# Kernel optimization log

Hardware: AMD Instinct MI355X
Metric: run time of the kernel (lower is better)

The kernel has to match this reference:

```python
import jax, jax.numpy as jnp
import numpy as np

B, CS, CD = 2, 128, 128
SRC = (8, 16, 16)
DST = (16, 32, 32)
G, K = 8, 3           # deform_groups, dcn_kernel
K3 = K ** 3


def setup_inputs() -> dict:
    key = jax.random.key(0)
    k1, k2, k3, k4 = jax.random.split(key, 4)
    feat_1x_src = jax.random.normal(k1, (B, CS) + SRC, dtype=jnp.float32)
    feat_2x_dst = jax.random.normal(k2, (B, CD) + DST, dtype=jnp.float32)
    # 1x1 Conv3d (bias=False): in = CD + CS = 256, out = K^3 * 3 * G = 648
    w_offset = jax.random.normal(k3, (K3 * 3 * G, CD + CS), dtype=jnp.float32) * 0.02
    # DeformConv3D weight: [Cout, Cin, K, K, K], no bias
    w_dcn = jax.random.normal(k4, (CD, CS, K, K, K), dtype=jnp.float32) * 0.05
    return {"feat_1x_src": feat_1x_src, "feat_2x_dst": feat_2x_dst,
            "w_offset": w_offset, "w_dcn": w_dcn}


def _trilinear_gather(x_flat, z, y, x, Di, Hi, Wi):
    """Zero-padded trilinear sampling.
    x_flat: [B,G,Cg,Din*Hin*Win]; z,y,x: [B,G,P] float coords. -> [B,G,Cg,P]"""
    z0 = jnp.floor(z); y0 = jnp.floor(y); x0 = jnp.floor(x)
    fz = z - z0; fy = y - y0; fx = x - x0
    z0i = z0.astype(jnp.int32); y0i = y0.astype(jnp.int32); x0i = x0.astype(jnp.int32)
    acc = jnp.zeros(x_flat.shape[:3] + (z.shape[-1],), x_flat.dtype)
    for dz in (0, 1):
        wz = fz if dz else 1.0 - fz
        iz = z0i + dz
        for dy in (0, 1):
            wy = fy if dy else 1.0 - fy
            iy = y0i + dy
            for dx in (0, 1):
                wx = fx if dx else 1.0 - fx
                ix = x0i + dx
                valid = ((iz >= 0) & (iz < Di) & (iy >= 0) & (iy < Hi)
                         & (ix >= 0) & (ix < Wi))
                idx = (jnp.clip(iz, 0, Di - 1) * (Hi * Wi)
                       + jnp.clip(iy, 0, Hi - 1) * Wi
                       + jnp.clip(ix, 0, Wi - 1))
                val = jnp.take_along_axis(x_flat, idx[:, :, None, :], axis=-1)
                acc = acc + val * (wz * wy * wx * valid)[:, :, None, :]
    return acc


def reference(feat_1x_src, feat_2x_dst, w_offset, w_dcn):
    b, cs = feat_1x_src.shape[:2]
    D, H, W = feat_2x_dst.shape[2:]
    cd = w_dcn.shape[0]
    # F.interpolate trilinear, align_corners=False (half-pixel == jax.image.resize)
    feat_up = jax.image.resize(feat_1x_src, (b, cs, D, H, W), method="trilinear")
    # 1x1 offset conv on concat([dst, 2*up])
    cat = jnp.concatenate([feat_2x_dst, feat_up * 2.0], axis=1)
    offset = jnp.einsum("bcdhw,oc->bodhw", cat, w_offset)
    # offsets: [B, G, K3, 3(z,y,x), D, H, W]
    off = offset.reshape(b, G, K3, 3, D, H, W)
    P = D * H * W
    Cg = cs // G
    x_flat = feat_up.reshape(b, G, Cg, P)
    dd, hh, ww = jnp.meshgrid(jnp.arange(D, dtype=jnp.float32),
                              jnp.arange(H, dtype=jnp.float32),
                              jnp.arange(W, dtype=jnp.float32), indexing="ij")
    pad = (K - 1) // 2
    taps = [(kz - pad, ky - pad, kx - pad)
            for kz in range(K) for ky in range(K) for kx in range(K)]
    samples = []
    for k, (kz, ky, kx) in enumerate(taps):
        z = (dd[None, None] + kz + off[:, :, k, 0]).reshape(b, G, P)
        y = (hh[None, None] + ky + off[:, :, k, 1]).reshape(b, G, P)
        x = (ww[None, None] + kx + off[:, :, k, 2]).reshape(b, G, P)
        samples.append(_trilinear_gather(x_flat, z, y, x, D, H, W).reshape(b, cs, P))
    samp = jnp.stack(samples, axis=2)           # [B, Cin, K3, P]
    wk = w_dcn.reshape(cd, cs, K3)
    out = jnp.einsum("bckp,ock->bop", samp, wk).reshape(b, cd, D, H, W)
    return jax.nn.relu(out)
```

## Files before the change

kernel.cpp:

```cpp
#include <hip/hip_runtime.h>
#include <hip/hip_fp16.h>
#include <math.h>

#define BB   2
#define CSN  128
#define CDN  128
#define SD   8
#define SH   16
#define SW   16
#define DD   16
#define DH   32
#define DW   32
#define PP   (DD*DH*DW)
#define GG   8
#define K3   27
#define OO   648

typedef _Float16 half8 __attribute__((ext_vector_type(8)));
typedef float f32x4 __attribute__((ext_vector_type(4)));

__global__ __launch_bounds__(256) void prep_kernel(
    const float* __restrict__ src, const float* __restrict__ wof,
    const float* __restrict__ wdcn, half8* __restrict__ uph8,
    half8* __restrict__ woxg, half8* __restrict__ wtx2)
{
    __shared__ float slab[2 * 8 * 16 * 17];
    const int bid = blockIdx.x;
    const int tid = threadIdx.x;

    if (bid < 512) {
        const int zo = bid & 15, pl = bid >> 4;
        const int h = pl & 1, g = (pl >> 1) & 7, b = pl >> 4;
        const int z0 = (zo - 1) >> 1;
        const float fz = (zo & 1) ? 0.25f : 0.75f;
        {
            const int zi = tid >> 7, cc = (tid >> 4) & 7, y = tid & 15;
            const int zsrc = min(max(z0 + zi, 0), SD - 1);
            const float* srow = src +
                (((size_t)(b * CSN + g * 16 + h * 8 + cc) * SD + zsrc) * SH + y) * SW;
            float* drow = &slab[((zi * 8 + cc) * 16 + y) * 17];
            *(float4*)(drow)      = *(const float4*)(srow);
            *(float4*)(drow + 4)  = *(const float4*)(srow + 4);
            *(float4*)(drow + 8)  = *(const float4*)(srow + 8);
            *(float4*)(drow + 12) = *(const float4*)(srow + 12);
        }
        __syncthreads();

        const float wz0 = 1.f - fz, wz1 = fz;
#pragma unroll 1
        for (int i = 0; i < 4; ++i) {
            const int pp = tid + i * 256;
            const int yo = pp >> 5, xo = pp & 31;
            const int y0 = (yo - 1) >> 1;
            const float fy = (yo & 1) ? 0.25f : 0.75f;
            const int ys0 = max(y0, 0), ys1 = min(y0 + 1, SH - 1);
            const int x0 = (xo - 1) >> 1;
            const float fx = (xo & 1) ? 0.25f : 0.75f;
            const int xs0 = max(x0, 0), xs1 = min(x0 + 1, SW - 1);
            const float w00 = (1.f - fy) * (1.f - fx), w01 = (1.f - fy) * fx;
            const float w10 = fy * (1.f - fx),         w11 = fy * fx;
            const int a00 = ys0 * 17 + xs0, a01 = ys0 * 17 + xs1;
            const int a10 = ys1 * 17 + xs0, a11 = ys1 * 17 + xs1;

            half8 hv;
#pragma unroll
            for (int cc = 0; cc < 8; ++cc) {
                const float* pa = &slab[(cc * 16) * 17];
                const float* pb = &slab[((8 + cc) * 16) * 17];
                const float s0 = w00 * pa[a00] + w01 * pa[a01]
                               + w10 * pa[a10] + w11 * pa[a11];
                const float s1 = w00 * pb[a00] + w01 * pb[a01]
                               + w10 * pb[a10] + w11 * pb[a11];
                hv[cc] = (_Float16)(wz0 * s0 + wz1 * s1);
            }
            uph8[(size_t)pl * PP + zo * 1024 + pp] = hv;
        }
    } else if (bid < 608) {
        const int i = (bid - 512) * 256 + tid;
        const int q = i & 3, lo = (i >> 2) & 15;
        const int t6 = i >> 6;
        const int ot = t6 % 6;
        const int gc0 = t6 / 6;
        const int c0 = gc0 & 7, g = gc0 >> 3;
        const int m = ot * 16 + lo;
        half8 hv;
#pragma unroll
        for (int j = 0; j < 8; ++j) hv[j] = (_Float16)0.0f;
        if (m < 81) {
            const int o = g * 81 + m;
            const int c = c0 * 32 + q * 8;
            const float sc = (c >= 128) ? 2.0f : 1.0f;
            const float* wr = wof + (size_t)o * 256 + c;
#pragma unroll
            for (int j = 0; j < 8; ++j) hv[j] = (_Float16)(wr[j] * sc);
        }
        woxg[i] = hv;
    } else {
        const int i = (bid - 608) * 256 + tid;
        const int q = i & 3, lo = (i >> 2) & 15, ot = (i >> 6) & 7;
        const int gp = i >> 9;
        const int pair = gp % 14, g = gp / 14;
        const int tap = pair * 2 + (q >> 1);
        half8 hv;
#pragma unroll
        for (int j = 0; j < 8; ++j) hv[j] = (_Float16)0.0f;
        if (tap < K3) {
            const int o = ot * 16 + lo;
            const int cb = g * 16 + (q & 1) * 8;
            const float* wr = wdcn + ((size_t)(o * CSN + cb)) * K3 + tap;
#pragma unroll
            for (int j = 0; j < 8; ++j) hv[j] = (_Float16)wr[(size_t)j * K3];
        }
        wtx2[i] = hv;
    }
}

#define REGB_OFF 32768
#define SH2_OFF  61568
#define LDS_TOTAL 78976
#define SROW 68

__global__ __launch_bounds__(512, 4) void mega_kernel(
    const float* __restrict__ dst, const float4* __restrict__ up4,
    const half8* __restrict__ woxg, const half8* __restrict__ wtx2,
    float* __restrict__ out)
{
    __shared__ __align__(16) char ldsraw[LDS_TOTAL];
    half8* catx = (half8*)ldsraw;
    char* regB = ldsraw + REGB_OFF;
    _Float16* offls = (_Float16*)(ldsraw + SH2_OFF);
    half8* sampx = (half8*)(ldsraw + SH2_OFF);

    const int tid = threadIdx.x;
    const int b = blockIdx.y;
    const int cb = blockIdx.x;
    const int X4 = (cb & 7) << 2, Y4 = ((cb >> 3) & 7) << 2, Z4 = (cb >> 6) << 2;

    {
        const int co = tid >> 4, pq = tid & 15;
        const int cz = pq >> 2, cy = pq & 3;
        const int pbase = ((Z4 + cz) << 10) + ((Y4 + cy) << 5) + X4;
        if (co < 16) {
            const int c = co * 8;
            const float* dp = dst + ((size_t)(b * CDN + c) << 14) + pbase;
            float vv[32];
#pragma unroll
            for (int j = 0; j < 8; ++j)
                *(float4*)&vv[j * 4] = *(const float4*)(dp + ((size_t)j << 14));
#pragma unroll
            for (int i = 0; i < 4; ++i) {
                half8 hh;
#pragma unroll
                for (int j = 0; j < 8; ++j) hh[j] = (_Float16)vv[j * 4 + i];
                catx[co * 64 + pq * 4 + i] = hh;
            }
        } else {
            const int g2 = (co - 16) >> 1, oct = (co - 16) & 1;
            const half8* u8 = (const half8*)up4;
            const size_t base =
                ((size_t)((b * GG + g2) * 2 + oct) << 14) + pbase;
#pragma unroll
            for (int i = 0; i < 4; ++i)
                catx[co * 64 + pq * 4 + i] = u8[base + i];
        }
    }

    const int w = tid >> 6, l = tid & 63, lo = l & 15, q = l >> 4;
    const int t2 = w >> 1, h = w & 1;
    const int tp = l;
    const int cz = tp >> 4, cy = (tp >> 2) & 3, cx = tp & 3;
    const int zoA = Z4 + cz, yoA = Y4 + cy, xoA = X4 + cx;

    f32x4 acc[4];
#pragma unroll
    for (int ps = 0; ps < 4; ++ps) acc[ps] = (f32x4){0.f, 0.f, 0.f, 0.f};

#pragma unroll 1
    for (int g = 0; g < 8; ++g) {
        __syncthreads();

#pragma unroll 1
        for (int c = tid; c < 1800; c += 512) {
            const int hf = c & 1;
            const int v = c >> 1;
            const int zz = v / 100, r2 = v - zz * 100;
            const int yy = r2 / 10, xx = r2 - yy * 10;
            const int vz = min(max(Z4 - 3 + zz, 0), DD - 1);
            const int vy = min(max(Y4 - 3 + yy, 0), DH - 1);
            const int vx = min(max(X4 - 3 + xx, 0), DW - 1);
            const float4 val =
                up4[(size_t)((b * GG + g) * 2 + hf) * PP +
                    (vz << 10) + (vy << 5) + vx];
            const int sw = (xx + yy + zz + hf) & 1;
            *(float4*)(regB + v * 32 + sw * 16) = val;
        }

        if (w < 6) {
            f32x4 a[4];
#pragma unroll
            for (int ps = 0; ps < 4; ++ps) a[ps] = (f32x4){0.f, 0.f, 0.f, 0.f};
#pragma unroll
            for (int c0 = 0; c0 < 8; ++c0) {
                const half8 A =
                    woxg[(size_t)((((g * 8 + c0) * 6 + w) * 16 + lo) * 4 + q)];
#pragma unroll
                for (int ps = 0; ps < 4; ++ps) {
                    const half8 B = catx[(c0 * 4 + q) * 64 + ps * 16 + lo];
                    a[ps] = __builtin_amdgcn_mfma_f32_16x16x32_f16(A, B, a[ps], 0, 0, 0);
                }
            }
#pragma unroll
            for (int ps = 0; ps < 4; ++ps) {
#pragma unroll
                for (int r = 0; r < 4; ++r) {
                    const int m = w * 16 + q * 4 + r;
                    if (m < 81)
                        offls[m * 64 + ps * 16 + lo] = (_Float16)a[ps][r];
                }
            }
        }
        __syncthreads();

        float offv[7][3];
#pragma unroll
        for (int r = 0; r < 7; ++r) {
            const int tap = r * 4 + t2;
            if (tap < K3) {
#pragma unroll
                for (int c = 0; c < 3; ++c)
                    offv[r][c] = (float)offls[(tap * 3 + c) * 64 + tp];
            }
        }
        __syncthreads();

#pragma unroll
        for (int r = 0; r < 7; ++r) {
            half8* dbuf = sampx + (r & 1) * 544;
            const int tap = r * 4 + t2;
            if (tap < K3) {
                const int kz = tap / 9 - 1;
                const int ky = (tap / 3) % 3 - 1;
                const int kx = (tap % 3) - 1;
                const float z = (float)(zoA + kz) + offv[r][0];
                const float y = (float)(yoA + ky) + offv[r][1];
                const float x = (float)(xoA + kx) + offv[r][2];
                const float zf = floorf(z), yf = floorf(y), xf = floorf(x);
                const float fz = z - zf, fy = y - yf, fx = x - xf;
                const int z0i = (int)zf, y0i = (int)yf, x0i = (int)xf;

                const float wz0 = ((unsigned)z0i < DD) ? 1.f - fz : 0.f;
                const float wz1 = ((unsigned)(z0i + 1) < DD) ? fz : 0.f;
                const float wy0 = ((unsigned)y0i < DH) ? 1.f - fy : 0.f;
                const float wy1 = ((unsigned)(y0i + 1) < DH) ? fy : 0.f;
                const float wx0 = ((unsigned)x0i < DW) ? 1.f - fx : 0.f;
                const float wx1 = ((unsigned)(x0i + 1) < DW) ? fx : 0.f;
                float wcs[8];
                wcs[0] = wz0 * wy0 * wx0; wcs[1] = wz0 * wy0 * wx1;
                wcs[2] = wz0 * wy1 * wx0; wcs[3] = wz0 * wy1 * wx1;
                wcs[4] = wz1 * wy0 * wx0; wcs[5] = wz1 * wy0 * wx1;
                wcs[6] = wz1 * wy1 * wx0; wcs[7] = wz1 * wy1 * wx1;

                const int sz0 = z0i - (Z4 - 3);
                const int sy0 = y0i - (Y4 - 3);
                const int sx0 = x0i - (X4 - 3);

                __align__(16) __half2 acch[4];
#pragma unroll
                for (int rr = 0; rr < 4; ++rr) acch[rr] = __floats2half2_rn(0.f, 0.f);

                if ((unsigned)sz0 <= 7u && (unsigned)sy0 <= 8u &&
                    (unsigned)sx0 <= 8u) {
                    const int v000 = (sz0 * 10 + sy0) * 10 + sx0;
                    const int s0 = (sx0 + sy0 + sz0 + h) & 1;
                    const int s1 = s0 ^ 1;
                    const int vox[8] = {v000,       v000 + 1,
                                        v000 + 10,  v000 + 11,
                                        v000 + 100, v000 + 101,
                                        v000 + 110, v000 + 111};
                    const int sws[8] = {s0, s1, s1, s0, s1, s0, s0, s1};
                    half8 hv[8];
#pragma unroll
                    for (int ci = 0; ci < 8; ++ci)
                        hv[ci] = *(const half8*)(regB + vox[ci] * 32 + sws[ci] * 16);
#pragma unroll
                    for (int ci = 0; ci < 8; ++ci) {
                        const __half2 wh = __float2half2_rn(wcs[ci]);
                        const __half2* h2 = (const __half2*)&hv[ci];
#pragma unroll
                        for (int rr = 0; rr < 4; ++rr)
                            acch[rr] = __hfma2(h2[rr], wh, acch[rr]);
                    }
                } else {
                    const int iz0 = min(max(z0i, 0), DD - 1);
                    const int iz1 = min(max(z0i + 1, 0), DD - 1);
                    const int iy0 = min(max(y0i, 0), DH - 1);
                    const int iy1 = min(max(y0i + 1, 0), DH - 1);
                    const int ix0 = min(max(x0i, 0), DW - 1);
                    const int ix1 = min(max(x0i + 1, 0), DW - 1);
                    const int v000 = (iz0 << 10) + (iy0 << 5) + ix0;
                    const int dzo = (iz1 - iz0) << 10;
                    const int dyo = (iy1 - iy0) << 5;
                    const int dxo = ix1 - ix0;
                    const int vox[8] = {v000,             v000 + dxo,
                                        v000 + dyo,       v000 + dyo + dxo,
                                        v000 + dzo,       v000 + dzo + dxo,
                                        v000 + dzo + dyo, v000 + dzo + dyo + dxo};
                    const float4* baseF =
                        up4 + (size_t)((b * GG + g) * 2 + h) * PP;
#pragma unroll
                    for (int ci = 0; ci < 8; ++ci) {
                        const float4 u = baseF[vox[ci]];
                        const __half2 wh = __float2half2_rn(wcs[ci]);
                        const __half2* h2 = (const __half2*)&u;
#pragma unroll
                        for (int rr = 0; rr < 4; ++rr)
                            acch[rr] = __hfma2(h2[rr], wh, acch[rr]);
                    }
                }
                dbuf[(t2 * 2 + h) * SROW + tp + (tp >> 4)] = *(half8*)&acch[0];
            }
            __syncthreads();

#pragma unroll
            for (int p = 0; p < 2; ++p) {
                const half8 A = wtx2[(size_t)(
                    (((g * 14 + r * 2 + p) * 8 + w) * 16 + lo) * 4 + q)];
#pragma unroll
                for (int ps = 0; ps < 4; ++ps) {
                    const half8 B = dbuf[(p * 4 + q) * SROW + ps * 17 + lo];
                    acc[ps] = __builtin_amdgcn_mfma_f32_16x16x32_f16(A, B, acc[ps], 0, 0, 0);
                }
            }
        }
    }

#pragma unroll
    for (int ps = 0; ps < 4; ++ps) {
        const int zo = Z4 + ps, yo = Y4 + ((lo >> 2) & 3), xo = X4 + (lo & 3);
        const int paddr = (zo << 10) + (yo << 5) + xo;
#pragma unroll
        for (int r = 0; r < 4; ++r) {
            const int o = w * 16 + q * 4 + r;
            out[((size_t)(b * CDN + o) << 14) + paddr] = fmaxf(acc[ps][r], 0.f);
        }
    }
}

extern "C" void kernel_launch(void* const* d_in, const int* in_sizes, int n_in,
                              void* d_out, int out_size, void* d_ws, size_t ws_size,
                              hipStream_t stream)
{
    const float* src1x = (const float*)d_in[0];
    const float* dst2x = (const float*)d_in[1];
    const float* w_off = (const float*)d_in[2];
    const float* w_dcn = (const float*)d_in[3];
    float* out = (float*)d_out;

    char* ws = (char*)d_ws;
    half8* uph8 = (half8*)(ws);
    half8* woxg = (half8*)(ws + 8388608);
    half8* wtx2 = (half8*)(ws + 8781824);

    prep_kernel<<<dim3(832), dim3(256), 0, stream>>>(
        src1x, w_off, w_dcn, uph8, woxg, wtx2);
    mega_kernel<<<dim3(256, BB), dim3(512), 0, stream>>>(
        dst2x, (const float4*)uph8, woxg, wtx2, out);
}
```

Before: 207.9 us.

## Drop LDS halo staging of upsampled features; gather trilinear taps from global

Removes the per-group cooperative load of a 10x10x8 halo region of upsampled features into LDS and the fast/slow path branch, so every trilinear corner is now read straight from global memory (L1/L2). This shrinks LDS use from about 79KB to about 51KB and raises the launch-bounds occupancy hint from 4 to 6. The catx rows are padded to 66 entries to cut LDS bank conflicts. The trade-off is more global and cache traffic and longer gather latency per sample, in exchange for higher occupancy, fewer instructions and no halo load stage before each group.

```diff
diff --git a/kernel.cpp b/kernel.cpp
--- a/kernel.cpp
+++ b/kernel.cpp
@@ -115,19 +115,18 @@
     }
 }
 
-#define REGB_OFF 32768
-#define SH2_OFF  61568
-#define LDS_TOTAL 78976
+#define CROW 66
+#define SH2_OFF  33792
+#define LDS_TOTAL 51200
 #define SROW 68
 
-__global__ __launch_bounds__(512, 4) void mega_kernel(
+__global__ __launch_bounds__(512, 6) void mega_kernel(
     const float* __restrict__ dst, const float4* __restrict__ up4,
     const half8* __restrict__ woxg, const half8* __restrict__ wtx2,
     float* __restrict__ out)
 {
     __shared__ __align__(16) char ldsraw[LDS_TOTAL];
     half8* catx = (half8*)ldsraw;
-    char* regB = ldsraw + REGB_OFF;
     _Float16* offls = (_Float16*)(ldsraw + SH2_OFF);
     half8* sampx = (half8*)(ldsraw + SH2_OFF);
 
@@ -152,7 +151,7 @@
                 half8 hh;
 #pragma unroll
                 for (int j = 0; j < 8; ++j) hh[j] = (_Float16)vv[j * 4 + i];
-                catx[co * 64 + pq * 4 + i] = hh;
+                catx[co * CROW + pq * 4 + i] = hh;
             }
         } else {
             const int g2 = (co - 16) >> 1, oct = (co - 16) & 1;
@@ -161,7 +160,7 @@
                 ((size_t)((b * GG + g2) * 2 + oct) << 14) + pbase;
 #pragma unroll
             for (int i = 0; i < 4; ++i)
-                catx[co * 64 + pq * 4 + i] = u8[base + i];
+                catx[co * CROW + pq * 4 + i] = u8[base + i];
         }
     }
 
@@ -179,22 +178,6 @@
     for (int g = 0; g < 8; ++g) {
         __syncthreads();
 
-#pragma unroll 1
-        for (int c = tid; c < 1800; c += 512) {
-            const int hf = c & 1;
-            const int v = c >> 1;
-            const int zz = v / 100, r2 = v - zz * 100;
-            const int yy = r2 / 10, xx = r2 - yy * 10;
-            const int vz = min(max(Z4 - 3 + zz, 0), DD - 1);
-            const int vy = min(max(Y4 - 3 + yy, 0), DH - 1);
-            const int vx = min(max(X4 - 3 + xx, 0), DW - 1);
-            const float4 val =
-                up4[(size_t)((b * GG + g) * 2 + hf) * PP +
-                    (vz << 10) + (vy << 5) + vx];
-            const int sw = (xx + yy + zz + hf) & 1;
-            *(float4*)(regB + v * 32 + sw * 16) = val;
-        }
-
         if (w < 6) {
             f32x4 a[4];
 #pragma unroll
@@ -205,7 +188,7 @@
                     woxg[(size_t)((((g * 8 + c0) * 6 + w) * 16 + lo) * 4 + q)];
 #pragma unroll
                 for (int ps = 0; ps < 4; ++ps) {
-                    const half8 B = catx[(c0 * 4 + q) * 64 + ps * 16 + lo];
+                    const half8 B = catx[(c0 * 4 + q) * CROW + ps * 16 + lo];
                     a[ps] = __builtin_amdgcn_mfma_f32_16x16x32_f16(A, B, a[ps], 0, 0, 0);
                 }
             }
@@ -260,62 +243,34 @@
                 wcs[4] = wz1 * wy0 * wx0; wcs[5] = wz1 * wy0 * wx1;
                 wcs[6] = wz1 * wy1 * wx0; wcs[7] = wz1 * wy1 * wx1;
 
-                const int sz0 = z0i - (Z4 - 3);
-                const int sy0 = y0i - (Y4 - 3);
-                const int sx0 = x0i - (X4 - 3);
+                const int iz0 = min(max(z0i, 0), DD - 1);
+                const int iz1 = min(max(z0i + 1, 0), DD - 1);
+                const int iy0 = min(max(y0i, 0), DH - 1);
+                const int iy1 = min(max(y0i + 1, 0), DH - 1);
+                const int ix0 = min(max(x0i, 0), DW - 1);
+                const int ix1 = min(max(x0i + 1, 0), DW - 1);
+                const int v000 = (iz0 << 10) + (iy0 << 5) + ix0;
+                const int dzo = (iz1 - iz0) << 10;
+                const int dyo = (iy1 - iy0) << 5;
+                const int dxo = ix1 - ix0;
+                const int vox[8] = {v000,             v000 + dxo,
+                                    v000 + dyo,       v000 + dyo + dxo,
+                                    v000 + dzo,       v000 + dzo + dxo,
+                                    v000 + dzo + dyo, v000 + dzo + dyo + dxo};
+                const float4* baseF =
+                    up4 + (size_t)((b * GG + g) * 2 + h) * PP;
 
                 __align__(16) __half2 acch[4];
 #pragma unroll
                 for (int rr = 0; rr < 4; ++rr) acch[rr] = __floats2half2_rn(0.f, 0.f);
-
-                if ((unsigned)sz0 <= 7u && (unsigned)sy0 <= 8u &&
-                    (unsigned)sx0 <= 8u) {
-                    const int v000 = (sz0 * 10 + sy0) * 10 + sx0;
-                    const int s0 = (sx0 + sy0 + sz0 + h) & 1;
-                    const int s1 = s0 ^ 1;
-                    const int vox[8] = {v000,       v000 + 1,
-                                        v000 + 10,  v000 + 11,
-                                        v000 + 100, v000 + 101,
-                                        v000 + 110, v000 + 111};
-                    const int sws[8] = {s0, s1, s1, s0, s1, s0, s0, s1};
-                    half8 hv[8];
-#pragma unroll
-                    for (int ci = 0; ci < 8; ++ci)
-                        hv[ci] = *(const half8*)(regB + vox[ci] * 32 + sws[ci] * 16);
-#pragma unroll
-                    for (int ci = 0; ci < 8; ++ci) {
-                        const __half2 wh = __float2half2_rn(wcs[ci]);
-                        const __half2* h2 = (const __half2*)&hv[ci];
-#pragma unroll
-                        for (int rr = 0; rr < 4; ++rr)
-                            acch[rr] = __hfma2(h2[rr], wh, acch[rr]);
-                    }
-                } else {
-                    const int iz0 = min(max(z0i, 0), DD - 1);
-                    const int iz1 = min(max(z0i + 1, 0), DD - 1);
-                    const int iy0 = min(max(y0i, 0), DH - 1);
-                    const int iy1 = min(max(y0i + 1, 0), DH - 1);
-                    const int ix0 = min(max(x0i, 0), DW - 1);
-                    const int ix1 = min(max(x0i + 1, 0), DW - 1);
-                    const int v000 = (iz0 << 10) + (iy0 << 5) + ix0;
-                    const int dzo = (iz1 - iz0) << 10;
-                    const int dyo = (iy1 - iy0) << 5;
-                    const int dxo = ix1 - ix0;
-                    const int vox[8] = {v000,             v000 + dxo,
-                                        v000 + dyo,       v000 + dyo + dxo,
-                                        v000 + dzo,       v000 + dzo + dxo,
-                                        v000 + dzo + dyo, v000 + dzo + dyo + dxo};
-                    const float4* baseF =
-                        up4 + (size_t)((b * GG + g) * 2 + h) * PP;
-#pragma unroll
-                    for (int ci = 0; ci < 8; ++ci) {
-                        const float4 u = baseF[vox[ci]];
-                        const __half2 wh = __float2half2_rn(wcs[ci]);
-                        const __half2* h2 = (const __half2*)&u;
-#pragma unroll
-                        for (int rr = 0; rr < 4; ++rr)
-                            acch[rr] = __hfma2(h2[rr], wh, acch[rr]);
-                    }
+#pragma unroll
+                for (int ci = 0; ci < 8; ++ci) {
+                    const float4 u = baseF[vox[ci]];
+                    const __half2 wh = __float2half2_rn(wcs[ci]);
+                    const __half2* h2 = (const __half2*)&u;
+#pragma unroll
+                    for (int rr = 0; rr < 4; ++rr)
+                        acch[rr] = __hfma2(h2[rr], wh, acch[rr]);
                 }
                 dbuf[(t2 * 2 + h) * SROW + tp + (tp >> 4)] = *(half8*)&acch[0];
             }
```

Result: slower. 354.0 us (+70.3%).

## Split deform groups across two blocks, shrink LDS halo, reduce partials in a new kernel

Applied to the files above, without the earlier changes.

The mega kernel now runs on a grid with a z-dimension of 2, and each block handles 4 of the 8 deform groups. Group-half 0 writes fp32 partial sums to out and group-half 1 writes fp16 partials to a workspace buffer. A new reduce kernel adds the two partials and applies the ReLU. The sampling halo shrinks from 10^3 to 9^3 voxels, and the upsampled half of the concatenated input is read straight from global memory instead of LDS. Together these cut LDS use and allow 6 blocks per CU instead of 4. Block indices are also swizzled. This doubles the number of blocks, but it adds an extra kernel launch, extra global traffic for the partials, and some precision loss from storing one partial in fp16. The smaller halo sends more samples down the slow path.

```diff
diff --git a/kernel.cpp b/kernel.cpp
--- a/kernel.cpp
+++ b/kernel.cpp
@@ -115,32 +115,36 @@
     }
 }
 
-#define REGB_OFF 32768
-#define SH2_OFF  61568
-#define LDS_TOTAL 78976
-#define SROW 68
-
-__global__ __launch_bounds__(512, 4) void mega_kernel(
+#define REGB_OFF  16384
+#define SAMP_OFF  37120
+#define LDS_TOTAL 54272
+#define SROW 67
+#define DBUF_H8 536
+
+__global__ __launch_bounds__(512, 6) void mega_kernel(
     const float* __restrict__ dst, const float4* __restrict__ up4,
     const half8* __restrict__ woxg, const half8* __restrict__ wtx2,
-    float* __restrict__ out)
+    float* __restrict__ out, _Float16* __restrict__ p1)
 {
     __shared__ __align__(16) char ldsraw[LDS_TOTAL];
     half8* catx = (half8*)ldsraw;
     char* regB = ldsraw + REGB_OFF;
-    _Float16* offls = (_Float16*)(ldsraw + SH2_OFF);
-    half8* sampx = (half8*)(ldsraw + SH2_OFF);
+    _Float16* offls = (_Float16*)(ldsraw + SAMP_OFF);
+    half8* sampx = (half8*)(ldsraw + SAMP_OFF);
 
     const int tid = threadIdx.x;
     const int b = blockIdx.y;
-    const int cb = blockIdx.x;
+    const int gh = blockIdx.z;
+    const int cb0 = blockIdx.x;
+    const int cb = ((cb0 & 7) << 5) | (cb0 >> 3);
     const int X4 = (cb & 7) << 2, Y4 = ((cb >> 3) & 7) << 2, Z4 = (cb >> 6) << 2;
+    const half8* u8 = (const half8*)up4;
 
     {
         const int co = tid >> 4, pq = tid & 15;
-        const int cz = pq >> 2, cy = pq & 3;
-        const int pbase = ((Z4 + cz) << 10) + ((Y4 + cy) << 5) + X4;
         if (co < 16) {
+            const int cz = pq >> 2, cy = pq & 3;
+            const int pbase = ((Z4 + cz) << 10) + ((Y4 + cy) << 5) + X4;
             const int c = co * 8;
             const float* dp = dst + ((size_t)(b * CDN + c) << 14) + pbase;
             float vv[32];
@@ -154,14 +158,6 @@
                 for (int j = 0; j < 8; ++j) hh[j] = (_Float16)vv[j * 4 + i];
                 catx[co * 64 + pq * 4 + i] = hh;
             }
-        } else {
-            const int g2 = (co - 16) >> 1, oct = (co - 16) & 1;
-            const half8* u8 = (const half8*)up4;
-            const size_t base =
-                ((size_t)((b * GG + g2) * 2 + oct) << 14) + pbase;
-#pragma unroll
-            for (int i = 0; i < 4; ++i)
-                catx[co * 64 + pq * 4 + i] = u8[base + i];
         }
     }
 
@@ -170,24 +166,26 @@
     const int tp = l;
     const int cz = tp >> 4, cy = (tp >> 2) & 3, cx = tp & 3;
     const int zoA = Z4 + cz, yoA = Y4 + cy, xoA = X4 + cx;
+    const int voxA = ((Y4 + (lo >> 2)) << 5) + (X4 + (lo & 3));
 
     f32x4 acc[4];
 #pragma unroll
     for (int ps = 0; ps < 4; ++ps) acc[ps] = (f32x4){0.f, 0.f, 0.f, 0.f};
 
 #pragma unroll 1
-    for (int g = 0; g < 8; ++g) {
+    for (int gi = 0; gi < 4; ++gi) {
+        const int g = gh * 4 + gi;
         __syncthreads();
 
 #pragma unroll 1
-        for (int c = tid; c < 1800; c += 512) {
+        for (int c = tid; c < 1296; c += 512) {
             const int hf = c & 1;
             const int v = c >> 1;
-            const int zz = v / 100, r2 = v - zz * 100;
-            const int yy = r2 / 10, xx = r2 - yy * 10;
-            const int vz = min(max(Z4 - 3 + zz, 0), DD - 1);
-            const int vy = min(max(Y4 - 3 + yy, 0), DH - 1);
-            const int vx = min(max(X4 - 3 + xx, 0), DW - 1);
+            const int zz = v / 81, r2 = v - zz * 81;
+            const int yy = r2 / 9, xx = r2 - yy * 9;
+            const int vz = min(max(Z4 - 2 + zz, 0), DD - 1);
+            const int vy = min(max(Y4 - 2 + yy, 0), DH - 1);
+            const int vx = min(max(X4 - 2 + xx, 0), DW - 1);
             const float4 val =
                 up4[(size_t)((b * GG + g) * 2 + hf) * PP +
                     (vz << 10) + (vy << 5) + vx];
@@ -205,7 +203,14 @@
                     woxg[(size_t)((((g * 8 + c0) * 6 + w) * 16 + lo) * 4 + q)];
 #pragma unroll
                 for (int ps = 0; ps < 4; ++ps) {
-                    const half8 B = catx[(c0 * 4 + q) * 64 + ps * 16 + lo];
+                    half8 B;
+                    if (c0 < 4) {
+                        B = catx[(c0 * 4 + q) * 64 + ps * 16 + lo];
+                    } else {
+                        const int o8 = c0 * 4 + q - 16;
+                        B = u8[((size_t)((b * GG + (o8 >> 1)) * 2 + (o8 & 1)) << 14)
+                               + ((Z4 + ps) << 10) + voxA];
+                    }
                     a[ps] = __builtin_amdgcn_mfma_f32_16x16x32_f16(A, B, a[ps], 0, 0, 0);
                 }
             }
@@ -235,7 +240,7 @@
 
 #pragma unroll
         for (int r = 0; r < 7; ++r) {
-            half8* dbuf = sampx + (r & 1) * 544;
+            half8* dbuf = sampx + (r & 1) * DBUF_H8;
             const int tap = r * 4 + t2;
             if (tap < K3) {
                 const int kz = tap / 9 - 1;
@@ -260,23 +265,23 @@
                 wcs[4] = wz1 * wy0 * wx0; wcs[5] = wz1 * wy0 * wx1;
                 wcs[6] = wz1 * wy1 * wx0; wcs[7] = wz1 * wy1 * wx1;
 
-                const int sz0 = z0i - (Z4 - 3);
-                const int sy0 = y0i - (Y4 - 3);
-                const int sx0 = x0i - (X4 - 3);
+                const int sz0 = z0i - (Z4 - 2);
+                const int sy0 = y0i - (Y4 - 2);
+                const int sx0 = x0i - (X4 - 2);
 
                 __align__(16) __half2 acch[4];
 #pragma unroll
                 for (int rr = 0; rr < 4; ++rr) acch[rr] = __floats2half2_rn(0.f, 0.f);
 
-                if ((unsigned)sz0 <= 7u && (unsigned)sy0 <= 8u &&
-                    (unsigned)sx0 <= 8u) {
-                    const int v000 = (sz0 * 10 + sy0) * 10 + sx0;
+                if ((unsigned)sz0 <= 6u && (unsigned)sy0 <= 7u &&
+                    (unsigned)sx0 <= 7u) {
+                    const int v000 = (sz0 * 9 + sy0) * 9 + sx0;
                     const int s0 = (sx0 + sy0 + sz0 + h) & 1;
                     const int s1 = s0 ^ 1;
-                    const int vox[8] = {v000,       v000 + 1,
-                                        v000 + 10,  v000 + 11,
-                                        v000 + 100, v000 + 101,
-                                        v000 + 110, v000 + 111};
+                    const int vox[8] = {v000,      v000 + 1,
+                                        v000 + 9,  v000 + 10,
+                                        v000 + 81, v000 + 82,
+                                        v000 + 90, v000 + 91};
                     const int sws[8] = {s0, s1, s1, s0, s1, s0, s0, s1};
                     half8 hv[8];
 #pragma unroll
@@ -341,9 +346,29 @@
 #pragma unroll
         for (int r = 0; r < 4; ++r) {
             const int o = w * 16 + q * 4 + r;
-            out[((size_t)(b * CDN + o) << 14) + paddr] = fmaxf(acc[ps][r], 0.f);
-        }
-    }
+            const size_t off = ((size_t)(b * CDN + o) << 14) + paddr;
+            if (gh == 0) out[off] = acc[ps][r];
+            else         p1[off]  = (_Float16)acc[ps][r];
+        }
+    }
+}
+
+__global__ __launch_bounds__(256) void reduce_kernel(
+    float* __restrict__ out, const half8* __restrict__ p1)
+{
+    const int i = blockIdx.x * 256 + threadIdx.x;
+    float* o = out + (size_t)i * 8;
+    float4 a0 = *(float4*)(o);
+    float4 a1 = *(float4*)(o + 4);
+    const half8 p = p1[i];
+    float4 r0, r1;
+#pragma unroll
+    for (int j = 0; j < 4; ++j) {
+        r0[j == 0 ? 0 : j] = fmaxf(a0[j == 0 ? 0 : j] + (float)p[j], 0.f);
+        r1[j == 0 ? 0 : j] = fmaxf(a1[j == 0 ? 0 : j] + (float)p[4 + j], 0.f);
+    }
+    *(float4*)(o)     = r0;
+    *(float4*)(o + 4) = r1;
 }
 
 extern "C" void kernel_launch(void* const* d_in, const int* in_sizes, int n_in,
@@ -360,9 +385,12 @@
     half8* uph8 = (half8*)(ws);
     half8* woxg = (half8*)(ws + 8388608);
     half8* wtx2 = (half8*)(ws + 8781824);
+    _Float16* p1 = (_Float16*)(ws + 9699328);
 
     prep_kernel<<<dim3(832), dim3(256), 0, stream>>>(
         src1x, w_off, w_dcn, uph8, woxg, wtx2);
-    mega_kernel<<<dim3(256, BB), dim3(512), 0, stream>>>(
-        dst2x, (const float4*)uph8, woxg, wtx2, out);
+    mega_kernel<<<dim3(256, BB, 2), dim3(512), 0, stream>>>(
+        dst2x, (const float4*)uph8, woxg, wtx2, out, p1);
+    reduce_kernel<<<dim3(2048), dim3(256), 0, stream>>>(
+        out, (const half8*)p1);
 }
```

New measurement: 357.5 us. +72.0%, slower.
